# Optimization experiments

Hardware: AMD Instinct MI355X
Metric: run time of the kernel (lower is better)

The kernel has to match this reference:

```python
import jax, jax.numpy as jnp
import numpy as np

N_USER = 50000
N_ITEM = 50000
E = 800000
D_IN = 256
H = 4
D_OUT = 32


def setup_inputs() -> dict:
    key = jax.random.key(0)
    ks = jax.random.split(key, 13)
    s = 0.05  # param init scale
    return {
        "feat_user": jax.random.normal(ks[0], (N_USER, D_IN), jnp.float32),
        "feat_item": jax.random.normal(ks[1], (N_ITEM, D_IN), jnp.float32),
        # relation 1: user -> item
        "src_r1": jax.random.randint(ks[2], (E,), 0, N_USER, jnp.int32),
        "dst_r1": jax.random.randint(ks[3], (E,), 0, N_ITEM, jnp.int32),
        # relation 2: item -> user
        "src_r2": jax.random.randint(ks[4], (E,), 0, N_ITEM, jnp.int32),
        "dst_r2": jax.random.randint(ks[5], (E,), 0, N_USER, jnp.int32),
        "fc_r1": jax.random.normal(ks[6], (D_IN, H * D_OUT), jnp.float32) * s,
        "attn_l_r1": jax.random.normal(ks[7], (H, D_OUT), jnp.float32) * s,
        "attn_r_r1": jax.random.normal(ks[8], (H, D_OUT), jnp.float32) * s,
        "fc_r2": jax.random.normal(ks[9], (D_IN, H * D_OUT), jnp.float32) * s,
        "attn_l_r2": jax.random.normal(ks[10], (H, D_OUT), jnp.float32) * s,
        "attn_r_r2": jax.random.normal(ks[11], (H, D_OUT), jnp.float32) * s,
        "loop_weight": jax.random.normal(ks[12], (D_IN, D_OUT), jnp.float32) * s,
    }


def _gat_conv(feat_src, feat_dst, src, dst, fc, attn_l, attn_r, n_dst):
    """DGL-style GATConv: LeakyReLU(0.2) scores, edge softmax over dst, scatter-sum, elu."""
    hs = (feat_src @ fc).reshape(-1, H, D_OUT)  # (Nsrc, H, D)
    hd = (feat_dst @ fc).reshape(-1, H, D_OUT)  # (Ndst, H, D)
    el = jnp.sum(hs * attn_l, axis=-1)  # (Nsrc, H)
    er = jnp.sum(hd * attn_r, axis=-1)  # (Ndst, H)
    e = jax.nn.leaky_relu(el[src] + er[dst], 0.2)  # (E, H)
    # numerically stable segment softmax over dst neighborhoods
    emax = jax.ops.segment_max(e, dst, num_segments=n_dst)  # (Ndst, H)
    emax = jnp.where(jnp.isfinite(emax), emax, 0.0)  # zero-in-degree guard
    ex = jnp.exp(e - emax[dst])  # (E, H)
    denom = jax.ops.segment_sum(ex, dst, num_segments=n_dst)  # (Ndst, H)
    msg = ex[:, :, None] * hs[src]  # (E, H, D)
    agg = jax.ops.segment_sum(msg, dst, num_segments=n_dst)  # (Ndst, H, D)
    out = agg / jnp.maximum(denom, 1e-9)[:, :, None]
    return jax.nn.elu(out)


def reference(feat_user, feat_item, src_r1, dst_r1, src_r2, dst_r2,
              fc_r1, attn_l_r1, attn_r_r1, fc_r2, attn_l_r2, attn_r_r2,
              loop_weight):
    # HeteroGraphConv: each dst ntype receives one relation here (sum-agg trivial)
    h_item = _gat_conv(feat_user, feat_item, src_r1, dst_r1,
                       fc_r1, attn_l_r1, attn_r_r1, N_ITEM)
    h_user = _gat_conv(feat_item, feat_user, src_r2, dst_r2,
                       fc_r2, attn_l_r2, attn_r_r2, N_USER)
    # self-loop fusion + wrapper activation (dropout=0 is identity)
    h_item = jax.nn.elu(h_item + (feat_item @ loop_weight)[:, None, :])
    h_user = jax.nn.elu(h_user + (feat_user @ loop_weight)[:, None, :])
    return jnp.stack([h_user, h_item])  # (2, 50000, H, D_OUT)
```

## Files before the change

kernel.cpp:

```cpp
#include <hip/hip_runtime.h>
#include <hip/hip_bf16.h>
#include <cstdint>

#define NU 50000
#define NI 50000
#define NN 50000
#define EE 800000
#define DIN 256
#define NH 4
#define DOUT 32
#define HD 128
#define WC 176
#define NB 196
#define NBR 200
#define NBLK 400
#define EPB 4000
#define SCAP 6144
#define PACKB 352
#define WCAP 128

typedef __attribute__((ext_vector_type(8))) short short8;
typedef __attribute__((ext_vector_type(4))) float f32x4;
typedef __attribute__((ext_vector_type(2))) float f32x2;

__device__ __forceinline__ float leakyf(float x){ return x > 0.f ? x : 0.2f*x; }
__device__ __forceinline__ float eluf(float x){ return x > 0.f ? x : __expf(x) - 1.f; }
__device__ __forceinline__ unsigned short f2bf(float x){
  unsigned u = __float_as_uint(x);
  return (unsigned short)((u + 0x7FFFu + ((u >> 16) & 1u)) >> 16);
}
__device__ __forceinline__ float bf2f(unsigned short b){
  return __uint_as_float(((unsigned)b) << 16);
}
__device__ __forceinline__ float bflo(unsigned r){ return __uint_as_float(r << 16); }
__device__ __forceinline__ float bfhi(unsigned r){ return __uint_as_float(r & 0xffff0000u); }
__device__ __forceinline__ unsigned pk2(float x, float y){
  __hip_bfloat162 b = __float22bfloat162_rn(make_float2(x, y));
  union { __hip_bfloat162 b2; unsigned u; } c; c.b2 = b; return c.u;
}
__device__ __forceinline__ unsigned char f2fp8(float v){
  int pk = __builtin_amdgcn_cvt_pk_fp8_f32(v, v, 0, false);
  return (unsigned char)(pk & 0xff);
}
__device__ __forceinline__ void gload_lds16(const float* g, float* l) {
  __builtin_amdgcn_global_load_lds(
      (const __attribute__((address_space(1))) void*)g,
      (__attribute__((address_space(3))) void*)l, 16, 0, 0);
}

__global__ __launch_bounds__(256) void pack_bhist_k(
    const float* __restrict__ fc_r1, const float* __restrict__ al_r1,
    const float* __restrict__ ar_r1,
    const float* __restrict__ fc_r2, const float* __restrict__ al_r2,
    const float* __restrict__ ar_r2,
    const float* __restrict__ loopw,
    unsigned short* __restrict__ WtU, unsigned short* __restrict__ WtI,
    const int* __restrict__ d1, const int* __restrict__ d2,
    int* __restrict__ bhist) {
  __shared__ int hcnt[NB];
  int b = blockIdx.x;
  if (b < PACKB) {
    int side = b >= (PACKB/2);
    int bb = side ? b - (PACKB/2) : b;
    const float* fc_a = side ? fc_r2 : fc_r1;
    const float* al_a = side ? al_r2 : al_r1;
    const float* fc_b = side ? fc_r1 : fc_r2;
    const float* ar_b = side ? ar_r1 : ar_r2;
    unsigned short* Wt = side ? WtI : WtU;
    int t = bb*256 + threadIdx.x;
    if (t >= WC*DIN) return;
    int c = t >> 8, k = t & 255;
    float v = 0.f;
    if (c < HD) v = fc_a[k*HD + c];
    else if (c < HD+DOUT) v = loopw[k*DOUT + (c-HD)];
    else if (c < HD+DOUT+NH) {
      int h = c - (HD+DOUT); float s = 0.f;
      for (int dd = 0; dd < DOUT; ++dd) s += fc_a[k*HD + h*DOUT + dd] * al_a[h*DOUT + dd];
      v = s;
    } else if (c < HD+DOUT+2*NH) {
      int h = c - (HD+DOUT+NH); float s = 0.f;
      for (int dd = 0; dd < DOUT; ++dd) s += fc_b[k*HD + h*DOUT + dd] * ar_b[h*DOUT + dd];
      v = s;
    }
    Wt[t] = f2bf(v);
  } else {
    int blk = b - PACKB;
    int t = threadIdx.x;
    for (int i = t; i < NB; i += 256) hcnt[i] = 0;
    __syncthreads();
    int rel = blk >= NBR;
    const int* dd = rel ? d2 : d1;
    int e0 = (rel ? blk - NBR : blk) * EPB;
    for (int i = t; i < EPB; i += 256) atomicAdd(&hcnt[dd[e0+i] >> 8], 1);
    __syncthreads();
    for (int i = t; i < NB; i += 256) bhist[blk*NB + i] = hcnt[i];
  }
}

__global__ __launch_bounds__(512) void gemm_mfma(const float* __restrict__ Au,
                                                 const float* __restrict__ Ai,
                                                 const unsigned short* __restrict__ WtUp,
                                                 const unsigned short* __restrict__ WtIp,
                                                 unsigned char* __restrict__ hsbU8,
                                                 unsigned char* __restrict__ hsbI8,
                                                 unsigned short* __restrict__ loopbU,
                                                 unsigned short* __restrict__ loopbI,
                                                 unsigned short* __restrict__ elbU,
                                                 unsigned short* __restrict__ elbI,
                                                 float* __restrict__ erbU,
                                                 float* __restrict__ erbI) {
  int side = blockIdx.y;
  const float* A = side ? Ai : Au;
  const unsigned short* Wt = side ? WtIp : WtUp;
  unsigned char* hsb8 = side ? hsbI8 : hsbU8;
  unsigned short* loopb = side ? loopbI : loopbU;
  unsigned short* elb = side ? elbI : elbU;
  float* erb = side ? erbI : erbU;
  const int M = NN;

  __shared__ __align__(16) float As[2][128*32];
  __shared__ __align__(16) unsigned short Ws[2][176*40];
  int t = threadIdx.x;
  int bm = blockIdx.x * 128;
  int w = t >> 6, l = t & 63;
  int r16 = l & 15, g4 = l >> 4;
  f32x4 acc[11];
  #pragma unroll
  for (int f = 0; f < 11; ++f) acc[f] = (f32x4){0.f,0.f,0.f,0.f};

  int wc0 = t >> 2, woff0 = (t & 3) * 8;
  int wc1 = (t + 512) >> 2, woff1 = (t & 3) * 8;

  int r0 = w*8 + (l >> 3);
  int r1 = 64 + r0;
  int c0 = (l & 7) ^ (r0 & 7);
  int c1 = (l & 7) ^ (r1 & 7);
  int rs0 = bm + r0; if (rs0 >= M) rs0 = M - 1;
  int rs1 = bm + r1; if (rs1 >= M) rs1 = M - 1;
  const float* ga0 = A + (size_t)rs0*DIN + c0*4;
  const float* ga1 = A + (size_t)rs1*DIN + c1*4;

  uint4 wa, wb;
  auto loadW = [&](int k0) {
    wa = *(const uint4*)(Wt + wc0*DIN + k0 + woff0);
    if (t < 192) wb = *(const uint4*)(Wt + wc1*DIN + k0 + woff1);
  };
  auto storeW = [&](int buf) {
    *(uint4*)&Ws[buf][wc0*40 + woff0] = wa;
    if (t < 192) *(uint4*)&Ws[buf][wc1*40 + woff1] = wb;
  };
  auto issueA = [&](int kt, int buf) {
    gload_lds16(ga0 + kt*32, &As[buf][w*256]);
    gload_lds16(ga1 + kt*32, &As[buf][2048 + w*256]);
  };

  issueA(0, 0);
  loadW(0); storeW(0);
  #pragma unroll
  for (int kt = 0; kt < 8; ++kt) {
    int cur = kt & 1;
    if (kt < 7) loadW((kt + 1) * 32);
    __syncthreads();
    if (kt < 7) issueA(kt + 1, cur ^ 1);
    int R = w*16 + r16;
    int pc0 = (2*g4) ^ (R & 7);
    float4 fa = *(const float4*)&As[cur][R*32 + pc0*4];
    float4 fb = *(const float4*)&As[cur][R*32 + (pc0 ^ 1)*4];
    uint4 au;
    au.x = pk2(fa.x, fa.y); au.y = pk2(fa.z, fa.w);
    au.z = pk2(fb.x, fb.y); au.w = pk2(fb.z, fb.w);
    short8 a = *(short8*)&au;
    #pragma unroll
    for (int f = 0; f < 11; ++f) {
      short8 b = *(const short8*)&Ws[cur][(f*16 + r16)*40 + g4*8];
      acc[f] = __builtin_amdgcn_mfma_f32_16x16x32_bf16(a, b, acc[f], 0, 0, 0);
    }
    if (kt < 7) storeW(cur ^ 1);
  }
  #pragma unroll
  for (int f = 0; f < 11; ++f) {
    int c = f*16 + r16;
    #pragma unroll
    for (int r = 0; r < 4; ++r) {
      int row = bm + w*16 + g4*4 + r;
      if (row >= M) continue;
      float v = acc[f][r];
      if (c < HD) hsb8[(size_t)row*HD + c] = f2fp8(v);
      else if (c < HD+DOUT) loopb[(size_t)row*DOUT + (c-HD)] = f2bf(v);
      else if (c < HD+DOUT+NH) elb[(size_t)row*NH + (c-(HD+DOUT))] = f2bf(v);
      else if (c < HD+DOUT+2*NH) erb[(size_t)row*NH + (c-(HD+DOUT+NH))] = v;
    }
  }
}

__global__ __launch_bounds__(256) void btot_k(const int* __restrict__ bhist,
                                              int* __restrict__ bucketbase,
                                              int* __restrict__ offs) {
  int rel = blockIdx.x, t = threadIdx.x;
  int tot = 0;
  if (t < NB)
    for (int blk = 0; blk < NBR; ++blk) tot += bhist[(rel*NBR + blk)*NB + t];
  int lane = t & 63, wv = t >> 6;
  __shared__ int ws[4];
  int x = tot;
  #pragma unroll
  for (int st = 1; st < 64; st <<= 1) { int y = __shfl_up(x, st); if (lane >= st) x += y; }
  if (lane == 63) ws[wv] = x;
  __syncthreads();
  int add = 0;
  for (int ww = 0; ww < wv; ++ww) add += ws[ww];
  int exc = x - tot + add;
  if (t < NB) bucketbase[rel*(NB+1) + t] = exc;
  if (t == 0) {
    bucketbase[rel*(NB+1) + NB] = EE;
    offs[rel*(NN+1) + NN] = EE;
  }
}

__global__ __launch_bounds__(256) void bscan_k(const int* __restrict__ bucketbase,
                                               int* __restrict__ bhist) {
  int gb = blockIdx.x, t = threadIdx.x;
  int rel = gb >= NB, b = rel ? gb - NB : gb;
  int base = rel*EE + bucketbase[rel*(NB+1) + b];
  int v = (t < NBR) ? bhist[(rel*NBR + t)*NB + b] : 0;
  int lane = t & 63, wv = t >> 6;
  __shared__ int ws[4];
  int x = v;
  #pragma unroll
  for (int st = 1; st < 64; st <<= 1) { int y = __shfl_up(x, st); if (lane >= st) x += y; }
  if (lane == 63) ws[wv] = x;
  __syncthreads();
  int add = base;
  for (int ww = 0; ww < wv; ++ww) add += ws[ww];
  int exc = x - v + add;
  if (t < NBR) bhist[(rel*NBR + t)*NB + b] = exc;
}

__global__ __launch_bounds__(256) void bscat_k(const int* __restrict__ s1, const int* __restrict__ d1,
                                               const int* __restrict__ s2, const int* __restrict__ d2,
                                               const int* __restrict__ bhist,
                                               unsigned* __restrict__ binned) {
  __shared__ int cur[NB];
  int blk = blockIdx.x, t = threadIdx.x;
  int rel = blk >= NBR;
  const int* ssrc = rel ? s2 : s1;
  const int* dd   = rel ? d2 : d1;
  int e0 = (rel ? blk - NBR : blk) * EPB;
  for (int i = t; i < NB; i += 256) cur[i] = bhist[blk*NB + i];
  __syncthreads();
  for (int i = t; i < EPB; i += 256) {
    int d = dd[e0+i], s = ssrc[e0+i];
    int pos = atomicAdd(&cur[d >> 8], 1);
    binned[pos] = (unsigned)s | ((unsigned)(d & 255) << 16);
  }
}

__global__ __launch_bounds__(256) void fine_k(const unsigned* __restrict__ binned,
                                              const int* __restrict__ bucketbase,
                                              int* __restrict__ offs,
                                              unsigned short* __restrict__ sorted1,
                                              unsigned short* __restrict__ sorted2) {
  __shared__ int cnt[256];
  __shared__ int cur[256];
  __shared__ int ws[4];
  __shared__ unsigned short stag[SCAP];
  int b = blockIdx.x, rel = blockIdx.y, t = threadIdx.x;
  unsigned short* sorted = rel ? sorted2 : sorted1;
  int d0 = b << 8;
  int nd = min(256, NN - d0);
  int base = bucketbase[rel*(NB+1) + b];
  int total = bucketbase[rel*(NB+1) + b + 1] - base;
  cnt[t] = 0;
  __syncthreads();
  const unsigned* srcp = binned + (size_t)rel*EE + base;
  for (int i = t; i < total; i += 256) atomicAdd(&cnt[srcp[i] >> 16], 1);
  __syncthreads();
  int v = cnt[t];
  int lane = t & 63, wv = t >> 6;
  int x = v;
  #pragma unroll
  for (int st = 1; st < 64; st <<= 1) { int y = __shfl_up(x, st); if (lane >= st) x += y; }
  if (lane == 63) ws[wv] = x;
  __syncthreads();
  int add = 0;
  for (int ww = 0; ww < wv; ++ww) add += ws[ww];
  int exc = x - v + add;
  cur[t] = exc;
  if (t < nd) offs[rel*(NN+1) + d0 + t] = base + exc;
  __syncthreads();
  for (int i = t; i < total; i += 256) {
    unsigned e = srcp[i];
    int pos = atomicAdd(&cur[e >> 16], 1);
    if (pos < SCAP) stag[pos] = (unsigned short)(e & 0xffffu);
  }
  __syncthreads();
  for (int i = t; i < total; i += 256)
    sorted[base + i] = stag[i];
}

__global__ __launch_bounds__(256) void agg_k(const unsigned char* __restrict__ hsbU8,
                                             const unsigned char* __restrict__ hsbI8,
                                             const unsigned short* __restrict__ loopbU,
                                             const unsigned short* __restrict__ loopbI,
                                             const unsigned short* __restrict__ elbU,
                                             const unsigned short* __restrict__ elbI,
                                             const float* __restrict__ erbU,
                                             const float* __restrict__ erbI,
                                             const int* __restrict__ offs,
                                             const unsigned short* __restrict__ sorted1,
                                             const unsigned short* __restrict__ sorted2,
                                             float* __restrict__ out) {
  __shared__ float wlds[4][WCAP*NH];
  int wvid = threadIdx.x >> 6;
  float* mywl = wlds[wvid];
  int gw = __builtin_amdgcn_readfirstlane((blockIdx.x*blockDim.x + threadIdx.x) >> 6);
  int rel = gw >= NN;
  int d = rel ? gw - NN : gw;
  const unsigned char* hsb8 = rel ? hsbI8 : hsbU8;
  const unsigned short* lpb = rel ? loopbU : loopbI;
  const unsigned short* el_src = rel ? elbI : elbU;
  const float*          er_dst = rel ? erbU : erbI;
  const int*   of = offs + rel*(NN+1);
  const unsigned short* ss = rel ? sorted2 : sorted1;
  float* o = (rel ? out : out + (size_t)NN*HD) + (size_t)d*HD;
  int l = threadIdx.x & 63;
  int beg = of[d], end = of[d+1];
  int deg = end - beg;

  int hp = l >> 4, q = l & 15;
  float rdn = 0.f, er = 0.f;
  if (deg > 0) {
    er = er_dst[(size_t)d*NH + hp];
    float dnp = 0.f;
    int c = 0;
    for (int p0 = beg; p0 < end; p0 += 16, ++c) {
      int p = p0 + q;
      if (p < end) {
        int s = (int)ss[p];
        float ex = __expf(leakyf(bf2f(el_src[(size_t)s*NH + hp]) + er));
        dnp += ex;
        if (c < (WCAP/16)) mywl[(p - beg)*NH + hp] = ex;
      }
    }
    #pragma unroll
    for (int st = 1; st < 16; st <<= 1) dnp += __shfl_xor(dnp, st);
    rdn = 1.f / dnp;
  }
  asm volatile("s_waitcnt lgkmcnt(0)" ::: "memory");

  int g = l >> 4, j = l & 15, h = j >> 2;
  int fastend = (deg > WCAP) ? (beg + WCAP) : end;
  float a0=0.f,a1=0.f,a2=0.f,a3=0.f,a4=0.f,a5=0.f,a6=0.f,a7=0.f;
  int p = beg;
  for (; p + 8 <= fastend; p += 8) {
    int sA = (int)ss[p + g];
    int sB = (int)ss[p + 4 + g];
    float wA = mywl[(p + g - beg)*NH + h];
    float wB = mywl[(p + 4 + g - beg)*NH + h];
    uint2 rA = *(const uint2*)&hsb8[(size_t)sA*HD + 8*j];
    uint2 rB = *(const uint2*)&hsb8[(size_t)sB*HD + 8*j];
    f32x2 f0 = __builtin_amdgcn_cvt_pk_f32_fp8(rA.x, false);
    f32x2 f1 = __builtin_amdgcn_cvt_pk_f32_fp8(rA.x, true);
    f32x2 f2 = __builtin_amdgcn_cvt_pk_f32_fp8(rA.y, false);
    f32x2 f3 = __builtin_amdgcn_cvt_pk_f32_fp8(rA.y, true);
    a0 = fmaf(wA, f0.x, a0); a1 = fmaf(wA, f0.y, a1);
    a2 = fmaf(wA, f1.x, a2); a3 = fmaf(wA, f1.y, a3);
    a4 = fmaf(wA, f2.x, a4); a5 = fmaf(wA, f2.y, a5);
    a6 = fmaf(wA, f3.x, a6); a7 = fmaf(wA, f3.y, a7);
    f32x2 g0 = __builtin_amdgcn_cvt_pk_f32_fp8(rB.x, false);
    f32x2 g1 = __builtin_amdgcn_cvt_pk_f32_fp8(rB.x, true);
    f32x2 g2 = __builtin_amdgcn_cvt_pk_f32_fp8(rB.y, false);
    f32x2 g3 = __builtin_amdgcn_cvt_pk_f32_fp8(rB.y, true);
    a0 = fmaf(wB, g0.x, a0); a1 = fmaf(wB, g0.y, a1);
    a2 = fmaf(wB, g1.x, a2); a3 = fmaf(wB, g1.y, a3);
    a4 = fmaf(wB, g2.x, a4); a5 = fmaf(wB, g2.y, a5);
    a6 = fmaf(wB, g3.x, a6); a7 = fmaf(wB, g3.y, a7);
  }
  for (; p < fastend; p += 4) {
    if (p + g < fastend) {
      int sA = (int)ss[p + g];
      float wA = mywl[(p + g - beg)*NH + h];
      uint2 rA = *(const uint2*)&hsb8[(size_t)sA*HD + 8*j];
      f32x2 f0 = __builtin_amdgcn_cvt_pk_f32_fp8(rA.x, false);
      f32x2 f1 = __builtin_amdgcn_cvt_pk_f32_fp8(rA.x, true);
      f32x2 f2 = __builtin_amdgcn_cvt_pk_f32_fp8(rA.y, false);
      f32x2 f3 = __builtin_amdgcn_cvt_pk_f32_fp8(rA.y, true);
      a0 = fmaf(wA, f0.x, a0); a1 = fmaf(wA, f0.y, a1);
      a2 = fmaf(wA, f1.x, a2); a3 = fmaf(wA, f1.y, a3);
      a4 = fmaf(wA, f2.x, a4); a5 = fmaf(wA, f2.y, a5);
      a6 = fmaf(wA, f3.x, a6); a7 = fmaf(wA, f3.y, a7);
    }
  }
  if (end > fastend) {
    float erg = __shfl(er, h*16);
    for (int pp = fastend; pp < end; ++pp) {
      int s = __builtin_amdgcn_readfirstlane((int)ss[pp]);
      float wv_ = __expf(leakyf(bf2f(el_src[(size_t)s*NH + h]) + erg));
      if (g == 0) {
        uint2 r = *(const uint2*)&hsb8[(size_t)s*HD + 8*j];
        f32x2 f0 = __builtin_amdgcn_cvt_pk_f32_fp8(r.x, false);
        f32x2 f1 = __builtin_amdgcn_cvt_pk_f32_fp8(r.x, true);
        f32x2 f2 = __builtin_amdgcn_cvt_pk_f32_fp8(r.y, false);
        f32x2 f3 = __builtin_amdgcn_cvt_pk_f32_fp8(r.y, true);
        a0 = fmaf(wv_, f0.x, a0); a1 = fmaf(wv_, f0.y, a1);
        a2 = fmaf(wv_, f1.x, a2); a3 = fmaf(wv_, f1.y, a3);
        a4 = fmaf(wv_, f2.x, a4); a5 = fmaf(wv_, f2.y, a5);
        a6 = fmaf(wv_, f3.x, a6); a7 = fmaf(wv_, f3.y, a7);
      }
    }
  }
  a0 += __shfl_xor(a0, 16); a0 += __shfl_xor(a0, 32);
  a1 += __shfl_xor(a1, 16); a1 += __shfl_xor(a1, 32);
  a2 += __shfl_xor(a2, 16); a2 += __shfl_xor(a2, 32);
  a3 += __shfl_xor(a3, 16); a3 += __shfl_xor(a3, 32);
  a4 += __shfl_xor(a4, 16); a4 += __shfl_xor(a4, 32);
  a5 += __shfl_xor(a5, 16); a5 += __shfl_xor(a5, 32);
  a6 += __shfl_xor(a6, 16); a6 += __shfl_xor(a6, 32);
  a7 += __shfl_xor(a7, 16); a7 += __shfl_xor(a7, 32);
  float rdng = __shfl(rdn, h*16);
  if (g == 0) {
    uint4 lp = *(const uint4*)&lpb[(size_t)d*DOUT + 8*(j & 3)];
    float4 v0, v1;
    v0.x = eluf(eluf(a0*rdng) + bflo(lp.x)); v0.y = eluf(eluf(a1*rdng) + bfhi(lp.x));
    v0.z = eluf(eluf(a2*rdng) + bflo(lp.y)); v0.w = eluf(eluf(a3*rdng) + bfhi(lp.y));
    v1.x = eluf(eluf(a4*rdng) + bflo(lp.z)); v1.y = eluf(eluf(a5*rdng) + bfhi(lp.z));
    v1.z = eluf(eluf(a6*rdng) + bflo(lp.w)); v1.w = eluf(eluf(a7*rdng) + bfhi(lp.w));
    *(float4*)&o[8*j] = v0;
    *(float4*)&o[8*j + 4] = v1;
  }
}

extern "C" void kernel_launch(void* const* d_in, const int* in_sizes, int n_in,
                              void* d_out, int out_size, void* d_ws, size_t ws_size,
                              hipStream_t stream) {
  const float* feat_user  = (const float*)d_in[0];
  const float* feat_item  = (const float*)d_in[1];
  const int*   src_r1     = (const int*)d_in[2];
  const int*   dst_r1     = (const int*)d_in[3];
  const int*   src_r2     = (const int*)d_in[4];
  const int*   dst_r2     = (const int*)d_in[5];
  const float* fc_r1      = (const float*)d_in[6];
  const float* attn_l_r1  = (const float*)d_in[7];
  const float* attn_r_r1  = (const float*)d_in[8];
  const float* fc_r2      = (const float*)d_in[9];
  const float* attn_l_r2  = (const float*)d_in[10];
  const float* attn_r_r2  = (const float*)d_in[11];
  const float* loopw      = (const float*)d_in[12];

  float* out = (float*)d_out;

  char* ws = (char*)d_ws;
  unsigned short* WtU   = (unsigned short*)ws;            ws += WC*DIN*2;
  unsigned short* WtI   = (unsigned short*)ws;            ws += WC*DIN*2;
  unsigned char*  hsbU8 = (unsigned char*)ws;             ws += (size_t)NU*HD;
  unsigned char*  hsbI8 = (unsigned char*)ws;             ws += (size_t)NI*HD;
  unsigned short* loopbU= (unsigned short*)ws;            ws += (size_t)NU*DOUT*2;
  unsigned short* loopbI= (unsigned short*)ws;            ws += (size_t)NI*DOUT*2;
  unsigned short* elbU  = (unsigned short*)ws;            ws += (size_t)NU*NH*2;
  unsigned short* elbI  = (unsigned short*)ws;            ws += (size_t)NI*NH*2;
  float*          erbU  = (float*)ws;                     ws += (size_t)NU*NH*4;
  float*          erbI  = (float*)ws;                     ws += (size_t)NI*NH*4;
  int*            offs  = (int*)ws;                       ws += 2*(NN+1)*4;
  int*            bktb  = (int*)ws;                       ws += 2*(NB+1)*4;
  int*            bhist = (int*)ws;                       ws += (size_t)NBLK*NB*4;
  unsigned*       binned= (unsigned*)ws;                  ws += (size_t)2*EE*4;
  unsigned short* sorted1=(unsigned short*)ws;            ws += (size_t)EE*2;
  unsigned short* sorted2=(unsigned short*)ws;            ws += (size_t)EE*2;

  pack_bhist_k<<<PACKB + NBLK, 256, 0, stream>>>(fc_r1, attn_l_r1, attn_r_r1,
                                                 fc_r2, attn_l_r2, attn_r_r2,
                                                 loopw, WtU, WtI,
                                                 dst_r1, dst_r2, bhist);
  btot_k<<<2, 256, 0, stream>>>(bhist, bktb, offs);
  bscan_k<<<2*NB, 256, 0, stream>>>(bktb, bhist);
  bscat_k<<<NBLK, 256, 0, stream>>>(src_r1, dst_r1, src_r2, dst_r2, bhist, binned);
  fine_k<<<dim3(NB,2), 256, 0, stream>>>(binned, bktb, offs, sorted1, sorted2);

  gemm_mfma<<<dim3((NN+127)/128, 2), 512, 0, stream>>>(feat_user, feat_item, WtU, WtI,
                                                       hsbU8, hsbI8, loopbU, loopbI,
                                                       elbU, elbI, erbU, erbI);

  agg_k<<<(2*NN*64)/256, 256, 0, stream>>>(hsbU8, hsbI8, loopbU, loopbI,
                                           elbU, elbI, erbU, erbI,
                                           offs, sorted1, sorted2, out);
}
```

Measured before the change: 144.0 us.

## Fuse edge bucket scatter into GEMM launch as extra grid row

Merges the bucket-scatter kernel into the MFMA GEMM kernel by adding a third grid row of blocks that perform the scatter while the other rows do the projection GEMM. Shared memory becomes a single pool that both roles carve up. The aim is to drop one launch and let the memory-bound scatter overlap with the compute-bound GEMM. In exchange the grid carries early-exit blocks, and scatter blocks now reserve the GEMM's full shared memory, which can reduce occupancy.

```diff
diff --git a/kernel.cpp b/kernel.cpp
--- a/kernel.cpp
+++ b/kernel.cpp
@@ -18,6 +18,7 @@
 #define SCAP 6144
 #define PACKB 352
 #define WCAP 128
+#define GEMMB 391
 
 typedef __attribute__((ext_vector_type(8))) short short8;
 typedef __attribute__((ext_vector_type(4))) float f32x4;
@@ -97,18 +98,78 @@
   }
 }
 
-__global__ __launch_bounds__(512) void gemm_mfma(const float* __restrict__ Au,
-                                                 const float* __restrict__ Ai,
-                                                 const unsigned short* __restrict__ WtUp,
-                                                 const unsigned short* __restrict__ WtIp,
-                                                 unsigned char* __restrict__ hsbU8,
-                                                 unsigned char* __restrict__ hsbI8,
-                                                 unsigned short* __restrict__ loopbU,
-                                                 unsigned short* __restrict__ loopbI,
-                                                 unsigned short* __restrict__ elbU,
-                                                 unsigned short* __restrict__ elbI,
-                                                 float* __restrict__ erbU,
-                                                 float* __restrict__ erbI) {
+__global__ __launch_bounds__(256) void btot_k(const int* __restrict__ bhist,
+                                              int* __restrict__ bucketbase,
+                                              int* __restrict__ offs) {
+  int rel = blockIdx.x, t = threadIdx.x;
+  int tot = 0;
+  if (t < NB)
+    for (int blk = 0; blk < NBR; ++blk) tot += bhist[(rel*NBR + blk)*NB + t];
+  int lane = t & 63, wv = t >> 6;
+  __shared__ int ws[4];
+  int x = tot;
+  #pragma unroll
+  for (int st = 1; st < 64; st <<= 1) { int y = __shfl_up(x, st); if (lane >= st) x += y; }
+  if (lane == 63) ws[wv] = x;
+  __syncthreads();
+  int add = 0;
+  for (int ww = 0; ww < wv; ++ww) add += ws[ww];
+  int exc = x - tot + add;
+  if (t < NB) bucketbase[rel*(NB+1) + t] = exc;
+  if (t == 0) {
+    bucketbase[rel*(NB+1) + NB] = EE;
+    offs[rel*(NN+1) + NN] = EE;
+  }
+}
+
+__global__ __launch_bounds__(256) void bscan_k(const int* __restrict__ bucketbase,
+                                               int* __restrict__ bhist) {
+  int gb = blockIdx.x, t = threadIdx.x;
+  int rel = gb >= NB, b = rel ? gb - NB : gb;
+  int base = rel*EE + bucketbase[rel*(NB+1) + b];
+  int v = (t < NBR) ? bhist[(rel*NBR + t)*NB + b] : 0;
+  int lane = t & 63, wv = t >> 6;
+  __shared__ int ws[4];
+  int x = v;
+  #pragma unroll
+  for (int st = 1; st < 64; st <<= 1) { int y = __shfl_up(x, st); if (lane >= st) x += y; }
+  if (lane == 63) ws[wv] = x;
+  __syncthreads();
+  int add = base;
+  for (int ww = 0; ww < wv; ++ww) add += ws[ww];
+  int exc = x - v + add;
+  if (t < NBR) bhist[(rel*NBR + t)*NB + b] = exc;
+}
+
+__global__ __launch_bounds__(512) void gemm_bscat_k(
+    const float* __restrict__ Au, const float* __restrict__ Ai,
+    const unsigned short* __restrict__ WtUp, const unsigned short* __restrict__ WtIp,
+    unsigned char* __restrict__ hsbU8, unsigned char* __restrict__ hsbI8,
+    unsigned short* __restrict__ loopbU, unsigned short* __restrict__ loopbI,
+    unsigned short* __restrict__ elbU, unsigned short* __restrict__ elbI,
+    float* __restrict__ erbU, float* __restrict__ erbI,
+    const int* __restrict__ s1, const int* __restrict__ d1,
+    const int* __restrict__ s2, const int* __restrict__ d2,
+    const int* __restrict__ bhist, unsigned* __restrict__ binned) {
+  __shared__ __align__(16) char pool[60928];
+  if (blockIdx.y == 2) {
+    if (blockIdx.x >= NBLK) return;
+    int* cur = (int*)pool;
+    int blk = blockIdx.x, t = threadIdx.x;
+    int rel = blk >= NBR;
+    const int* ssrc = rel ? s2 : s1;
+    const int* dd   = rel ? d2 : d1;
+    int e0 = (rel ? blk - NBR : blk) * EPB;
+    for (int i = t; i < NB; i += 512) cur[i] = bhist[blk*NB + i];
+    __syncthreads();
+    for (int i = t; i < EPB; i += 512) {
+      int d = dd[e0+i], s = ssrc[e0+i];
+      int pos = atomicAdd(&cur[d >> 8], 1);
+      binned[pos] = (unsigned)s | ((unsigned)(d & 255) << 16);
+    }
+    return;
+  }
+  if (blockIdx.x >= GEMMB) return;
   int side = blockIdx.y;
   const float* A = side ? Ai : Au;
   const unsigned short* Wt = side ? WtIp : WtUp;
@@ -118,8 +179,8 @@
   float* erb = side ? erbI : erbU;
   const int M = NN;
 
-  __shared__ __align__(16) float As[2][128*32];
-  __shared__ __align__(16) unsigned short Ws[2][176*40];
+  float* As = (float*)pool;
+  unsigned short* Wsp = (unsigned short*)(pool + 32768);
   int t = threadIdx.x;
   int bm = blockIdx.x * 128;
   int w = t >> 6, l = t & 63;
@@ -146,12 +207,12 @@
     if (t < 192) wb = *(const uint4*)(Wt + wc1*DIN + k0 + woff1);
   };
   auto storeW = [&](int buf) {
-    *(uint4*)&Ws[buf][wc0*40 + woff0] = wa;
-    if (t < 192) *(uint4*)&Ws[buf][wc1*40 + woff1] = wb;
+    *(uint4*)&Wsp[buf*7040 + wc0*40 + woff0] = wa;
+    if (t < 192) *(uint4*)&Wsp[buf*7040 + wc1*40 + woff1] = wb;
   };
   auto issueA = [&](int kt, int buf) {
-    gload_lds16(ga0 + kt*32, &As[buf][w*256]);
-    gload_lds16(ga1 + kt*32, &As[buf][2048 + w*256]);
+    gload_lds16(ga0 + kt*32, As + buf*4096 + w*256);
+    gload_lds16(ga1 + kt*32, As + buf*4096 + 2048 + w*256);
   };
 
   issueA(0, 0);
@@ -164,15 +225,15 @@
     if (kt < 7) issueA(kt + 1, cur ^ 1);
     int R = w*16 + r16;
     int pc0 = (2*g4) ^ (R & 7);
-    float4 fa = *(const float4*)&As[cur][R*32 + pc0*4];
-    float4 fb = *(const float4*)&As[cur][R*32 + (pc0 ^ 1)*4];
+    float4 fa = *(const float4*)&As[cur*4096 + R*32 + pc0*4];
+    float4 fb = *(const float4*)&As[cur*4096 + R*32 + (pc0 ^ 1)*4];
     uint4 au;
     au.x = pk2(fa.x, fa.y); au.y = pk2(fa.z, fa.w);
     au.z = pk2(fb.x, fb.y); au.w = pk2(fb.z, fb.w);
     short8 a = *(short8*)&au;
     #pragma unroll
     for (int f = 0; f < 11; ++f) {
-      short8 b = *(const short8*)&Ws[cur][(f*16 + r16)*40 + g4*8];
+      short8 b = *(const short8*)&Wsp[cur*7040 + (f*16 + r16)*40 + g4*8];
       acc[f] = __builtin_amdgcn_mfma_f32_16x16x32_bf16(a, b, acc[f], 0, 0, 0);
     }
     if (kt < 7) storeW(cur ^ 1);
@@ -190,68 +251,6 @@
       else if (c < HD+DOUT+NH) elb[(size_t)row*NH + (c-(HD+DOUT))] = f2bf(v);
       else if (c < HD+DOUT+2*NH) erb[(size_t)row*NH + (c-(HD+DOUT+NH))] = v;
     }
-  }
-}
-
-__global__ __launch_bounds__(256) void btot_k(const int* __restrict__ bhist,
-                                              int* __restrict__ bucketbase,
-                                              int* __restrict__ offs) {
-  int rel = blockIdx.x, t = threadIdx.x;
-  int tot = 0;
-  if (t < NB)
-    for (int blk = 0; blk < NBR; ++blk) tot += bhist[(rel*NBR + blk)*NB + t];
-  int lane = t & 63, wv = t >> 6;
-  __shared__ int ws[4];
-  int x = tot;
-  #pragma unroll
-  for (int st = 1; st < 64; st <<= 1) { int y = __shfl_up(x, st); if (lane >= st) x += y; }
-  if (lane == 63) ws[wv] = x;
-  __syncthreads();
-  int add = 0;
-  for (int ww = 0; ww < wv; ++ww) add += ws[ww];
-  int exc = x - tot + add;
-  if (t < NB) bucketbase[rel*(NB+1) + t] = exc;
-  if (t == 0) {
-    bucketbase[rel*(NB+1) + NB] = EE;
-    offs[rel*(NN+1) + NN] = EE;
-  }
-}
-
-__global__ __launch_bounds__(256) void bscan_k(const int* __restrict__ bucketbase,
-                                               int* __restrict__ bhist) {
-  int gb = blockIdx.x, t = threadIdx.x;
-  int rel = gb >= NB, b = rel ? gb - NB : gb;
-  int base = rel*EE + bucketbase[rel*(NB+1) + b];
-  int v = (t < NBR) ? bhist[(rel*NBR + t)*NB + b] : 0;
-  int lane = t & 63, wv = t >> 6;
-  __shared__ int ws[4];
-  int x = v;
-  #pragma unroll
-  for (int st = 1; st < 64; st <<= 1) { int y = __shfl_up(x, st); if (lane >= st) x += y; }
-  if (lane == 63) ws[wv] = x;
-  __syncthreads();
-  int add = base;
-  for (int ww = 0; ww < wv; ++ww) add += ws[ww];
-  int exc = x - v + add;
-  if (t < NBR) bhist[(rel*NBR + t)*NB + b] = exc;
-}
-
-__global__ __launch_bounds__(256) void bscat_k(const int* __restrict__ s1, const int* __restrict__ d1,
-                                               const int* __restrict__ s2, const int* __restrict__ d2,
-                                               const int* __restrict__ bhist,
-                                               unsigned* __restrict__ binned) {
-  __shared__ int cur[NB];
-  int blk = blockIdx.x, t = threadIdx.x;
-  int rel = blk >= NBR;
-  const int* ssrc = rel ? s2 : s1;
-  const int* dd   = rel ? d2 : d1;
-  int e0 = (rel ? blk - NBR : blk) * EPB;
-  for (int i = t; i < NB; i += 256) cur[i] = bhist[blk*NB + i];
-  __syncthreads();
-  for (int i = t; i < EPB; i += 256) {
-    int d = dd[e0+i], s = ssrc[e0+i];
-    int pos = atomicAdd(&cur[d >> 8], 1);
-    binned[pos] = (unsigned)s | ((unsigned)(d & 255) << 16);
   }
 }
 
@@ -473,12 +472,14 @@
                                                  dst_r1, dst_r2, bhist);
   btot_k<<<2, 256, 0, stream>>>(bhist, bktb, offs);
   bscan_k<<<2*NB, 256, 0, stream>>>(bktb, bhist);
-  bscat_k<<<NBLK, 256, 0, stream>>>(src_r1, dst_r1, src_r2, dst_r2, bhist, binned);
+
+  gemm_bscat_k<<<dim3(NBLK, 3), 512, 0, stream>>>(feat_user, feat_item, WtU, WtI,
+                                                  hsbU8, hsbI8, loopbU, loopbI,
+                                                  elbU, elbI, erbU, erbI,
+                                                  src_r1, dst_r1, src_r2, dst_r2,
+                                                  bhist, binned);
+
   fine_k<<<dim3(NB,2), 256, 0, stream>>>(binned, bktb, offs, sorted1, sorted2);
-
-  gemm_mfma<<<dim3((NN+127)/128, 2), 512, 0, stream>>>(feat_user, feat_item, WtU, WtI,
-                                                       hsbU8, hsbI8, loopbU, loopbI,
-                                                       elbU, elbI, erbU, erbI);
 
   agg_k<<<(2*NN*64)/256, 256, 0, stream>>>(hsbU8, hsbI8, loopbU, loopbI,
                                            elbU, elbI, erbU, erbI,
```

New measurement: 136.3 us. 5.3% less time.
